# Kernel optimization log

Hardware: AMD Instinct MI355X
Metric: run time of the kernel (lower is better)

The kernel has to match this reference:

```python
import jax, jax.numpy as jnp
import numpy as np

L, B, S, H = 13, 32, 128, 768   # encoder hidden states: layers, batch (hardcoded 32), seq, hidden
U = 32                          # num_gru_units
G = 2 * U                       # linear out dim / bidirectional GRU feature dim (64)
NL = 2                          # num_labels
EPS = 1e-3                      # keras LayerNormalization default epsilon


def setup_inputs() -> dict:
    key = jax.random.key(0)
    ks = jax.random.split(key, 10)
    def n(k, shape, scale=0.05):
        return (jax.random.normal(k, shape, jnp.float32) * scale).astype(jnp.float32)
    return {
        "xs": jax.random.normal(ks[0], (L, B, S, H), jnp.float32),
        "W_lin": n(ks[1], (H, G)),
        "b_lin": jnp.zeros((G,), jnp.float32),
        "ln_gamma": jnp.ones((G,), jnp.float32),
        "ln_beta": jnp.zeros((G,), jnp.float32),
        "Wk_f": n(ks[2], (G, 3 * U)),
        "Wr_f": n(ks[3], (U, 3 * U)),
        "b_f": jnp.zeros((2, 3 * U), jnp.float32),   # [input_bias, recurrent_bias] (reset_after=True)
        "Wk_b": n(ks[4], (G, 3 * U)),
        "Wr_b": n(ks[5], (U, 3 * U)),
        "b_b": jnp.zeros((2, 3 * U), jnp.float32),
        "W_cls": n(ks[6], (G, NL)),
        "b_cls": jnp.zeros((NL,), jnp.float32),
    }


def _layernorm(x, g, b):
    m = jnp.mean(x, axis=-1, keepdims=True)
    v = jnp.var(x, axis=-1, keepdims=True)
    return (x - m) * jax.lax.rsqrt(v + EPS) * g + b


def _gru_dir(seq, h0, Wk, Wr, bias):
    # Keras GRU v2 cell (reset_after=True). seq: [B,S,G], h0: [B,U]
    xp = jnp.einsum('bsg,gk->bsk', seq, Wk) + bias[0]  # [B,S,3U]
    def step(h, x_t):
        rec = h @ Wr + bias[1]                          # [B,3U]
        z = jax.nn.sigmoid(x_t[:, :U] + rec[:, :U])
        r = jax.nn.sigmoid(x_t[:, U:2 * U] + rec[:, U:2 * U])
        hh = jnp.tanh(x_t[:, 2 * U:] + r * rec[:, 2 * U:])
        hn = z * h + (1.0 - z) * hh
        return hn, hn
    hT, ys = jax.lax.scan(step, h0, jnp.swapaxes(xp, 0, 1))  # scan over time
    return jnp.swapaxes(ys, 0, 1), hT                        # [B,S,U], [B,U]


def reference(xs, W_lin, b_lin, ln_gamma, ln_beta,
              Wk_f, Wr_f, b_f, Wk_b, Wr_b, b_b, W_cls, b_cls):
    # _forward: loop over the 13 encoder hidden-state layers; the bidirectional
    # GRU output feeds back as a residual into the next layer's linear output.
    # Dropout layers are treated as identity (deterministic reference), under
    # which the 100-pass MC average equals a single pass.
    seq = jnp.zeros((B, S, G), xs.dtype)  # initial 'sequence' of zeros
    h1 = jnp.zeros((B, U), xs.dtype)      # initial_state=None -> zeros in keras
    h2 = jnp.zeros((B, U), xs.dtype)
    for i in range(L):
        x = _layernorm(xs[i] @ W_lin + b_lin + seq, ln_gamma, ln_beta)  # [B,S,G]
        out_f, h1 = _gru_dir(x, h1, Wk_f, Wr_f, b_f)
        out_b, h2 = _gru_dir(x[:, ::-1], h2, Wk_b, Wr_b, b_b)
        seq = jnp.concatenate([out_f, out_b[:, ::-1]], axis=-1)         # [B,S,2U]
    # tf.stack([h1,h2], -1) -> [B,U,2]; reshape [32,-1] interleaves fwd/bwd units
    hcat = jnp.stack([h1, h2], axis=-1).reshape(B, -1)                  # [B,2U]
    return jax.nn.softmax(hcat @ W_cls + b_cls, axis=-1)                # [B,NL]
```

## Files before the change

### kernel.cpp

```cpp
#include <hip/hip_runtime.h>
#include <hip/hip_fp16.h>

#define L_ 13
#define B_ 32
#define S_ 128
#define H_ 768
#define NU 32
#define GG 64
#define TU 96
#define LN_EPS 1e-3f
#define SEQ_ST 68
#define XT_ST 129
#define WK_ST 100
#define XPH_ST 100
#define K1f 1.4426950408889634f
#define K2f 2.8853900817779268f

#define DPP_X1  0xB1
#define DPP_X2  0x4E
#define DPP_X7  0x141
#define DPP_X15 0x140

typedef float v2f __attribute__((ext_vector_type(2)));
typedef _Float16 h2t __attribute__((ext_vector_type(2)));
typedef unsigned int uv2 __attribute__((ext_vector_type(2)));

union F4H8 { float4 f4; __half2 hh[4]; h2t h[4]; };
union FH2  { float f; __half2 hh; h2t h; };
union F2H2 { float2 f2; __half2 hh[2]; };

__device__ __forceinline__ void pkfma(v2f& a, v2f x, v2f w) {
    asm("v_pk_fma_f32 %0, %1, %2, %0" : "+v"(a) : "v"(x), "v"(w));
}
template <int CTRL>
__device__ __forceinline__ float dppf(float x) {
    return __int_as_float(__builtin_amdgcn_update_dpp(
        0, __float_as_int(x), CTRL, 0xF, 0xF, true));
}
__device__ __forceinline__ float pairsum16(float x) {
#if __has_builtin(__builtin_amdgcn_permlane16_swap)
    uv2 s = __builtin_amdgcn_permlane16_swap(
        __float_as_uint(x), __float_as_uint(x), false, false);
    return __uint_as_float(s.x) + __uint_as_float(s.y);
#else
    return x + __shfl_xor(x, 16);
#endif
}
__device__ __forceinline__ void poll_ge_dev(unsigned* p, unsigned tgt) {
    int gd = 0;
    while (__hip_atomic_load(p, __ATOMIC_ACQUIRE, __HIP_MEMORY_SCOPE_AGENT) < tgt) {
        __builtin_amdgcn_s_sleep(2);
        if (++gd > (1 << 22)) break;
    }
}

__global__ __launch_bounds__(512) void fused_kernel(
    const float* __restrict__ xs, const float* __restrict__ Wl,
    const float* __restrict__ bl,
    __half* __restrict__ lin_all, unsigned* __restrict__ lincnt,
    const float* __restrict__ Wr_f, const float* __restrict__ b_f,
    const float* __restrict__ Wr_b, const float* __restrict__ b_b,
    const float* __restrict__ Wk_f, const float* __restrict__ Wk_b,
    const float* __restrict__ ln_g, const float* __restrict__ ln_b,
    const float* __restrict__ W_cls, const float* __restrict__ b_cls,
    float* __restrict__ out)
{
    extern __shared__ float sm[];
    const int bid = blockIdx.x;
    const int t = threadIdx.x;

    if (bid >= B_) {
        const int tix = bid - B_;
        const int l = tix >> 5;
        const int bb = tix & 31;
        const size_t row0 = (size_t)(l * B_ + bb) * S_;
        __half2* sA2 = (__half2*)sm;
        __half2* sW2 = (__half2*)(sm + 32 * 132);

        const int rgrp = t & 31;
        const int cg = t >> 5;
        const int c0 = cg * 4;

        float acc[4][4];
        #pragma unroll
        for (int i = 0; i < 4; ++i)
            #pragma unroll
            for (int j = 0; j < 4; ++j) acc[i][j] = 0.f;

        for (int kt = 0; kt < H_; kt += 64) {
            #pragma unroll
            for (int i = 0; i < 4; ++i) {
                const int idx = t + 512 * i;
                const int r = idx >> 4, kq = idx & 15;
                float4 a = *(const float4*)&xs[(row0 + r) * H_ + kt + kq * 4];
                sA2[(2 * kq) * 132 + r]     = __floats2half2_rn(a.x, a.y);
                sA2[(2 * kq + 1) * 132 + r] = __floats2half2_rn(a.z, a.w);
            }
            {
                const int k2 = t >> 4, c4 = (t & 15) * 4;
                float4 w0 = *(const float4*)&Wl[(size_t)(kt + 2 * k2) * GG + c4];
                float4 w1 = *(const float4*)&Wl[(size_t)(kt + 2 * k2 + 1) * GG + c4];
                sW2[k2 * 68 + c4 + 0] = __floats2half2_rn(w0.x, w1.x);
                sW2[k2 * 68 + c4 + 1] = __floats2half2_rn(w0.y, w1.y);
                sW2[k2 * 68 + c4 + 2] = __floats2half2_rn(w0.z, w1.z);
                sW2[k2 * 68 + c4 + 3] = __floats2half2_rn(w0.w, w1.w);
            }
            __syncthreads();
            #pragma unroll 4
            for (int k2 = 0; k2 < 32; ++k2) {
                FH2 x0, x1, x2, x3;
                x0.hh = sA2[k2 * 132 + rgrp];
                x1.hh = sA2[k2 * 132 + rgrp + 32];
                x2.hh = sA2[k2 * 132 + rgrp + 64];
                x3.hh = sA2[k2 * 132 + rgrp + 96];
                F4H8 w; w.f4 = *(const float4*)&sW2[k2 * 68 + c0];
                #pragma unroll
                for (int m = 0; m < 4; ++m) {
                    acc[0][m] = __builtin_amdgcn_fdot2(x0.h, w.h[m], acc[0][m], false);
                    acc[1][m] = __builtin_amdgcn_fdot2(x1.h, w.h[m], acc[1][m], false);
                    acc[2][m] = __builtin_amdgcn_fdot2(x2.h, w.h[m], acc[2][m], false);
                    acc[3][m] = __builtin_amdgcn_fdot2(x3.h, w.h[m], acc[3][m], false);
                }
            }
            __syncthreads();
        }
        const float4 bv = *(const float4*)&bl[c0];
        #pragma unroll
        for (int i = 0; i < 4; ++i) {
            const int r = rgrp + 32 * i;
            F2H2 u;
            u.hh[0] = __floats2half2_rn(acc[i][0] + bv.x, acc[i][1] + bv.y);
            u.hh[1] = __floats2half2_rn(acc[i][2] + bv.z, acc[i][3] + bv.w);
            *(float2*)&lin_all[(row0 + r) * GG + c0] = u.f2;
        }
        __threadfence();
        __syncthreads();
        if (t == 0)
            __hip_atomic_fetch_add(&lincnt[l], 1u, __ATOMIC_RELEASE, __HIP_MEMORY_SCOPE_AGENT);
        return;
    }

    float*   seqb = sm;
    __half2* xt2  = (__half2*)(sm + 8704);
    __half2* wk2  = (__half2*)(sm + 8704 + 4128);
    __half*  xph  = (__half*)(sm + 8704 + 4128 + 6400);
    float*   hbf  = sm + 8704 + 4128 + 6400 + 12800;
    float*   hbb  = hbf + NU;

    const int b = bid;
    const int wave = t >> 6;
    const int lane = t & 63;
    const int v16 = lane & 15;
    const int b4 = (lane >> 4) & 1;
    const int b5 = (lane >> 5) & 1;
    const int ud = v16 + 16 * b5;

    for (int i = t; i < S_ * SEQ_ST; i += 512) seqb[i] = 0.f;
    for (int i = t; i < 2 * 32 * 96; i += 512) {
        const int d = i / 3072, rem = i - d * 3072, k2 = rem / 96, c = rem - k2 * 96;
        const float* W = d ? Wk_b : Wk_f;
        const float sc = (c >= 64) ? K2f : K1f;
        wk2[(d * 32 + k2) * WK_ST + c] =
            __floats2half2_rn(W[(2 * k2) * TU + c] * sc, W[(2 * k2 + 1) * TU + c] * sc);
    }

    v2f wz[8], wr_[8], wh[8];
    float h_store = 0.f, h_dot = 0.f, rbz2 = 0.f, rbr2 = 0.f, rbh2 = 0.f;
    if (wave < 2) {
        const float* Wr   = wave ? Wr_b : Wr_f;
        const float* bias = wave ? b_b  : b_f;
        const int ex[8] = {0, 2, 7, 5, 15, 13, 8, 10};
        const int ey[8] = {1, 3, 6, 4, 14, 12, 9, 11};
        const int BB = 16 * b4;
        #pragma unroll
        for (int m = 0; m < 8; ++m) {
            const int jx = BB + (v16 ^ ex[m]), jy = BB + (v16 ^ ey[m]);
            wz[m]  = v2f{ K1f * Wr[jx * TU + ud],          K1f * Wr[jy * TU + ud] };
            wr_[m] = v2f{ K1f * Wr[jx * TU + NU + ud],     K1f * Wr[jy * TU + NU + ud] };
            wh[m]  = v2f{ K2f * Wr[jx * TU + 2 * NU + ud], K2f * Wr[jy * TU + 2 * NU + ud] };
        }
        rbz2 = 0.5f * K1f * bias[TU + ud];
        rbr2 = 0.5f * K1f * bias[TU + NU + ud];
        rbh2 = 0.5f * K2f * bias[TU + 2 * NU + ud];
    }

    const int g8 = t >> 3;
    const int c8 = (t & 7) << 3;
    const int rgrp = t & 31;
    const int cg = t >> 5;
    const int dsel = cg >> 3;
    const int cc = (cg & 7) * 12;
    const float* bias0 = dsel ? b_b : b_f;
    const __half2* wkd = wk2 + dsel * 32 * WK_ST;
    __half* xpd = xph + dsel * (S_ * XPH_ST);
    float bsc[12];
    #pragma unroll
    for (int m = 0; m < 12; ++m)
        bsc[m] = bias0[cc + m] * ((cc + m >= 64) ? K2f : K1f);

    __syncthreads();

    for (int l = 0; l < L_; ++l) {
        const __half* linb = lin_all + (size_t)(l * B_ + b) * S_ * GG;

        if (t == 0) poll_ge_dev(&lincnt[l], 32u);
        __syncthreads();

        #pragma unroll
        for (int p = 0; p < 2; ++p) {
            const int r = g8 + 64 * p;
            F4H8 lu; lu.f4 = *(const float4*)&linb[(size_t)r * GG + c8];
            float4 s0 = *(const float4*)&seqb[r * SEQ_ST + c8];
            float4 s1 = *(const float4*)&seqb[r * SEQ_ST + c8 + 4];
            float2 l0 = __half22float2(lu.hh[0]);
            float2 l1 = __half22float2(lu.hh[1]);
            float2 l2 = __half22float2(lu.hh[2]);
            float2 l3 = __half22float2(lu.hh[3]);
            float v[8];
            v[0] = l0.x + s0.x; v[1] = l0.y + s0.y; v[2] = l1.x + s0.z; v[3] = l1.y + s0.w;
            v[4] = l2.x + s1.x; v[5] = l2.y + s1.y; v[6] = l3.x + s1.z; v[7] = l3.y + s1.w;
            float s = 0.f;
            #pragma unroll
            for (int j = 0; j < 8; ++j) s += v[j];
            #pragma unroll
            for (int off = 1; off < 8; off <<= 1) s += __shfl_xor(s, off);
            const float mean = s * 0.015625f;
            float q = 0.f;
            float d[8];
            #pragma unroll
            for (int j = 0; j < 8; ++j) { d[j] = v[j] - mean; q += d[j] * d[j]; }
            #pragma unroll
            for (int off = 1; off < 8; off <<= 1) q += __shfl_xor(q, off);
            const float rstd = rsqrtf(q * 0.015625f + LN_EPS);
            float4 g0 = *(const float4*)&ln_g[c8];
            float4 g1 = *(const float4*)&ln_g[c8 + 4];
            float4 b0 = *(const float4*)&ln_b[c8];
            float4 b1 = *(const float4*)&ln_b[c8 + 4];
            float x[8];
            x[0] = d[0] * rstd * g0.x + b0.x; x[1] = d[1] * rstd * g0.y + b0.y;
            x[2] = d[2] * rstd * g0.z + b0.z; x[3] = d[3] * rstd * g0.w + b0.w;
            x[4] = d[4] * rstd * g1.x + b1.x; x[5] = d[5] * rstd * g1.y + b1.y;
            x[6] = d[6] * rstd * g1.z + b1.z; x[7] = d[7] * rstd * g1.w + b1.w;
            #pragma unroll
            for (int j = 0; j < 4; ++j)
                xt2[(c8 / 2 + j) * XT_ST + r] = __floats2half2_rn(x[2 * j], x[2 * j + 1]);
        }
        __syncthreads();

        {
            float acc[4][12];
            #pragma unroll
            for (int m = 0; m < 12; ++m) {
                acc[0][m] = bsc[m]; acc[1][m] = bsc[m]; acc[2][m] = bsc[m]; acc[3][m] = bsc[m];
            }
            #pragma unroll 4
            for (int k2 = 0; k2 < 32; ++k2) {
                FH2 x0, x1, x2, x3;
                x0.hh = xt2[k2 * XT_ST + rgrp];
                x1.hh = xt2[k2 * XT_ST + rgrp + 32];
                x2.hh = xt2[k2 * XT_ST + rgrp + 64];
                x3.hh = xt2[k2 * XT_ST + rgrp + 96];
                F4H8 wa, wb, wc;
                wa.f4 = *(const float4*)&wkd[k2 * WK_ST + cc];
                wb.f4 = *(const float4*)&wkd[k2 * WK_ST + cc + 4];
                wc.f4 = *(const float4*)&wkd[k2 * WK_ST + cc + 8];
                #pragma unroll
                for (int m = 0; m < 4; ++m) {
                    acc[0][m]     = __builtin_amdgcn_fdot2(x0.h, wa.h[m], acc[0][m],     false);
                    acc[1][m]     = __builtin_amdgcn_fdot2(x1.h, wa.h[m], acc[1][m],     false);
                    acc[2][m]     = __builtin_amdgcn_fdot2(x2.h, wa.h[m], acc[2][m],     false);
                    acc[3][m]     = __builtin_amdgcn_fdot2(x3.h, wa.h[m], acc[3][m],     false);
                    acc[0][m + 4] = __builtin_amdgcn_fdot2(x0.h, wb.h[m], acc[0][m + 4], false);
                    acc[1][m + 4] = __builtin_amdgcn_fdot2(x1.h, wb.h[m], acc[1][m + 4], false);
                    acc[2][m + 4] = __builtin_amdgcn_fdot2(x2.h, wb.h[m], acc[2][m + 4], false);
                    acc[3][m + 4] = __builtin_amdgcn_fdot2(x3.h, wb.h[m], acc[3][m + 4], false);
                    acc[0][m + 8] = __builtin_amdgcn_fdot2(x0.h, wc.h[m], acc[0][m + 8], false);
                    acc[1][m + 8] = __builtin_amdgcn_fdot2(x1.h, wc.h[m], acc[1][m + 8], false);
                    acc[2][m + 8] = __builtin_amdgcn_fdot2(x2.h, wc.h[m], acc[2][m + 8], false);
                    acc[3][m + 8] = __builtin_amdgcn_fdot2(x3.h, wc.h[m], acc[3][m + 8], false);
                }
            }
            #pragma unroll
            for (int i = 0; i < 4; ++i) {
                const int r = rgrp + 32 * i;
                __half2* dst = (__half2*)&xpd[r * XPH_ST + cc];
                #pragma unroll
                for (int j = 0; j < 6; ++j)
                    dst[j] = __floats2half2_rn(acc[i][2 * j], acc[i][2 * j + 1]);
            }
        }
        __syncthreads();

        if (wave < 2) {
            const int dir = wave;
            const __half* xp = xph + dir * (S_ * XPH_ST);
            float* sq = seqb + dir * NU + (lane & 31);
            const int stp = dir ? -1 : 1;
            int s = dir ? (S_ - 1) : 0;
            const bool wl = (lane < 32);
            const bool fix = (b4 != b5);
            float xz = (float)xp[s * XPH_ST + ud];
            float xr = (float)xp[s * XPH_ST + 32 + ud];
            float xh = (float)xp[s * XPH_ST + 64 + ud];
            for (int st = 0; st < S_; ++st) {
                float nz = 0.f, nr = 0.f, nh = 0.f;
                if (st < S_ - 1) {
                    const int sn = s + stp;
                    nz = (float)xp[sn * XPH_ST + ud];
                    nr = (float)xp[sn * XPH_ST + 32 + ud];
                    nh = (float)xp[sn * XPH_ST + 64 + ud];
                }
                v2f ro[8];
                ro[0].x = h_store;                ro[0].y = dppf<DPP_X1>(h_store);
                ro[1].x = dppf<DPP_X2>(ro[0].x);  ro[1].y = dppf<DPP_X2>(ro[0].y);
                ro[2].x = dppf<DPP_X7>(ro[0].x);  ro[2].y = dppf<DPP_X7>(ro[0].y);
                ro[3].x = dppf<DPP_X7>(ro[1].x);  ro[3].y = dppf<DPP_X7>(ro[1].y);
                ro[4].x = dppf<DPP_X15>(ro[0].x); ro[4].y = dppf<DPP_X15>(ro[0].y);
                ro[5].x = dppf<DPP_X15>(ro[1].x); ro[5].y = dppf<DPP_X15>(ro[1].y);
                ro[6].x = dppf<DPP_X15>(ro[2].x); ro[6].y = dppf<DPP_X15>(ro[2].y);
                ro[7].x = dppf<DPP_X15>(ro[3].x); ro[7].y = dppf<DPP_X15>(ro[3].y);

                v2f aza = v2f{0.5f * xz + rbz2, 0.f}, azb = v2f{0.f, 0.f};
                v2f ara = v2f{0.5f * xr + rbr2, 0.f}, arb = v2f{0.f, 0.f};
                v2f aha = v2f{rbh2, 0.f},             ahb = v2f{0.f, 0.f};
                #pragma unroll
                for (int m = 0; m < 4; ++m) {
                    pkfma(aza, ro[m], wz[m]);      pkfma(azb, ro[m + 4], wz[m + 4]);
                    pkfma(ara, ro[m], wr_[m]);     pkfma(arb, ro[m + 4], wr_[m + 4]);
                    pkfma(aha, ro[m], wh[m]);      pkfma(ahb, ro[m + 4], wh[m + 4]);
                }
                v2f azs = aza + azb, ars = ara + arb, ahs = aha + ahb;
                const float pz = pairsum16(azs.x + azs.y);
                const float pr = pairsum16(ars.x + ars.y);
                const float ph = pairsum16(ahs.x + ahs.y);

                const float z  = __builtin_amdgcn_rcpf(1.0f + __builtin_amdgcn_exp2f(-pz));
                const float r  = __builtin_amdgcn_rcpf(1.0f + __builtin_amdgcn_exp2f(-pr));
                const float tt = xh + r * ph;
                const float et = __builtin_amdgcn_exp2f(-tt);
                const float hh = (1.0f - et) * __builtin_amdgcn_rcpf(1.0f + et);
                const float hn_raw = hh + z * (h_dot - hh);
                h_dot = hn_raw;
                uv2 s32 = __builtin_amdgcn_permlane32_swap(
                    __float_as_uint(hn_raw), __float_as_uint(hn_raw), false, false);
                const float v32 = wl ? __uint_as_float(s32.y) : __uint_as_float(s32.x);
                h_store = fix ? v32 : hn_raw;
                if (wl) sq[s * SEQ_ST] = h_store;
                s += stp; xz = nz; xr = nr; xh = nh;
            }
        }
        __syncthreads();
    }

    if (wave < 2 && lane < 32) (wave ? hbb : hbf)[lane & 31] = h_store;
    __syncthreads();
    if (t == 0) {
        float l0 = b_cls[0], l1 = b_cls[1];
        for (int j = 0; j < NU; ++j) {
            const float hf = hbf[j], hk = hbb[j];
            l0 += hf * W_cls[4 * j]     + hk * W_cls[4 * j + 2];
            l1 += hf * W_cls[4 * j + 1] + hk * W_cls[4 * j + 3];
        }
        const float m = fmaxf(l0, l1);
        const float e0 = __expf(l0 - m), e1 = __expf(l1 - m);
        const float inv = 1.0f / (e0 + e1);
        out[b * 2 + 0] = e0 * inv;
        out[b * 2 + 1] = e1 * inv;
    }
}

extern "C" void kernel_launch(void* const* d_in, const int* in_sizes, int n_in,
                              void* d_out, int out_size, void* d_ws, size_t ws_size,
                              hipStream_t stream) {
    const float* xs    = (const float*)d_in[0];
    const float* W_lin = (const float*)d_in[1];
    const float* b_lin = (const float*)d_in[2];
    const float* ln_g  = (const float*)d_in[3];
    const float* ln_b  = (const float*)d_in[4];
    const float* Wk_f  = (const float*)d_in[5];
    const float* Wr_f  = (const float*)d_in[6];
    const float* b_f   = (const float*)d_in[7];
    const float* Wk_b  = (const float*)d_in[8];
    const float* Wr_b  = (const float*)d_in[9];
    const float* b_b   = (const float*)d_in[10];
    const float* W_cls = (const float*)d_in[11];
    const float* b_cls = (const float*)d_in[12];
    float* out = (float*)d_out;

    char* ws = (char*)d_ws;
    __half* lin_all = (__half*)ws;
    unsigned* lincnt = (unsigned*)(ws + 6815744);

    hipMemsetAsync(lincnt, 0, 64, stream);

    const int smem = (8704 + 4128 + 6400 + 12800 + 64) * (int)sizeof(float);
    (void)hipFuncSetAttribute((const void*)fused_kernel,
                              hipFuncAttributeMaxDynamicSharedMemorySize, smem);

    fused_kernel<<<B_ + L_ * B_, 512, smem, stream>>>(
        xs, W_lin, b_lin, lin_all, lincnt,
        Wr_f, b_f, Wr_b, b_b, Wk_f, Wk_b, ln_g, ln_b, W_cls, b_cls, out);
}
```

Baseline: 613.5 us.

## Split fused producer/consumer kernel into separate linear and GRU-chain launches

Replaces the single persistent kernel, whose extra blocks computed the input projection and signalled per-layer counters that the GRU blocks polled, with two launches: a projection kernel over all layers, then the recurrent chain kernel. This removes the atomic polling, the counter memset and the fences, and the projection blocks no longer compete with the 32 chain blocks for resources. In exchange, the chain can no longer start layer 0 while later layers' projections are still being computed, so that overlap is lost and the full projection cost sits on the critical path.

```diff
diff --git a/kernel.cpp b/kernel.cpp
--- a/kernel.cpp
+++ b/kernel.cpp
@@ -46,18 +46,77 @@
     return x + __shfl_xor(x, 16);
 #endif
 }
-__device__ __forceinline__ void poll_ge_dev(unsigned* p, unsigned tgt) {
-    int gd = 0;
-    while (__hip_atomic_load(p, __ATOMIC_ACQUIRE, __HIP_MEMORY_SCOPE_AGENT) < tgt) {
-        __builtin_amdgcn_s_sleep(2);
-        if (++gd > (1 << 22)) break;
-    }
-}
-
-__global__ __launch_bounds__(512) void fused_kernel(
+
+__global__ __launch_bounds__(512) void lin2_kernel(
     const float* __restrict__ xs, const float* __restrict__ Wl,
-    const float* __restrict__ bl,
-    __half* __restrict__ lin_all, unsigned* __restrict__ lincnt,
+    const float* __restrict__ bl, __half* __restrict__ lin_all)
+{
+    __shared__ __half2 sA2[32 * 132];
+    __shared__ __half2 sW2[32 * 68];
+
+    const int tix = blockIdx.x;
+    const size_t row0 = (size_t)tix * S_;
+    const int t = threadIdx.x;
+    const int rgrp = t & 31;
+    const int cg = t >> 5;
+    const int c0 = cg * 4;
+
+    float acc[4][4];
+    #pragma unroll
+    for (int i = 0; i < 4; ++i)
+        #pragma unroll
+        for (int j = 0; j < 4; ++j) acc[i][j] = 0.f;
+
+    for (int kt = 0; kt < H_; kt += 64) {
+        #pragma unroll
+        for (int i = 0; i < 4; ++i) {
+            const int idx = t + 512 * i;
+            const int r = idx >> 4, kq = idx & 15;
+            float4 a = *(const float4*)&xs[(row0 + r) * H_ + kt + kq * 4];
+            sA2[(2 * kq) * 132 + r]     = __floats2half2_rn(a.x, a.y);
+            sA2[(2 * kq + 1) * 132 + r] = __floats2half2_rn(a.z, a.w);
+        }
+        {
+            const int k2 = t >> 4, c4 = (t & 15) * 4;
+            float4 w0 = *(const float4*)&Wl[(size_t)(kt + 2 * k2) * GG + c4];
+            float4 w1 = *(const float4*)&Wl[(size_t)(kt + 2 * k2 + 1) * GG + c4];
+            sW2[k2 * 68 + c4 + 0] = __floats2half2_rn(w0.x, w1.x);
+            sW2[k2 * 68 + c4 + 1] = __floats2half2_rn(w0.y, w1.y);
+            sW2[k2 * 68 + c4 + 2] = __floats2half2_rn(w0.z, w1.z);
+            sW2[k2 * 68 + c4 + 3] = __floats2half2_rn(w0.w, w1.w);
+        }
+        __syncthreads();
+        #pragma unroll 4
+        for (int k2 = 0; k2 < 32; ++k2) {
+            FH2 x0, x1, x2, x3;
+            x0.hh = sA2[k2 * 132 + rgrp];
+            x1.hh = sA2[k2 * 132 + rgrp + 32];
+            x2.hh = sA2[k2 * 132 + rgrp + 64];
+            x3.hh = sA2[k2 * 132 + rgrp + 96];
+            F4H8 w; w.f4 = *(const float4*)&sW2[k2 * 68 + c0];
+            #pragma unroll
+            for (int m = 0; m < 4; ++m) {
+                acc[0][m] = __builtin_amdgcn_fdot2(x0.h, w.h[m], acc[0][m], false);
+                acc[1][m] = __builtin_amdgcn_fdot2(x1.h, w.h[m], acc[1][m], false);
+                acc[2][m] = __builtin_amdgcn_fdot2(x2.h, w.h[m], acc[2][m], false);
+                acc[3][m] = __builtin_amdgcn_fdot2(x3.h, w.h[m], acc[3][m], false);
+            }
+        }
+        __syncthreads();
+    }
+    const float4 bv = *(const float4*)&bl[c0];
+    #pragma unroll
+    for (int i = 0; i < 4; ++i) {
+        const int r = rgrp + 32 * i;
+        F2H2 u;
+        u.hh[0] = __floats2half2_rn(acc[i][0] + bv.x, acc[i][1] + bv.y);
+        u.hh[1] = __floats2half2_rn(acc[i][2] + bv.z, acc[i][3] + bv.w);
+        *(float2*)&lin_all[(row0 + r) * GG + c0] = u.f2;
+    }
+}
+
+__global__ __launch_bounds__(512) void chain_kernel(
+    const __half* __restrict__ lin_all,
     const float* __restrict__ Wr_f, const float* __restrict__ b_f,
     const float* __restrict__ Wr_b, const float* __restrict__ b_b,
     const float* __restrict__ Wk_f, const float* __restrict__ Wk_b,
@@ -66,80 +125,6 @@
     float* __restrict__ out)
 {
     extern __shared__ float sm[];
-    const int bid = blockIdx.x;
-    const int t = threadIdx.x;
-
-    if (bid >= B_) {
-        const int tix = bid - B_;
-        const int l = tix >> 5;
-        const int bb = tix & 31;
-        const size_t row0 = (size_t)(l * B_ + bb) * S_;
-        __half2* sA2 = (__half2*)sm;
-        __half2* sW2 = (__half2*)(sm + 32 * 132);
-
-        const int rgrp = t & 31;
-        const int cg = t >> 5;
-        const int c0 = cg * 4;
-
-        float acc[4][4];
-        #pragma unroll
-        for (int i = 0; i < 4; ++i)
-            #pragma unroll
-            for (int j = 0; j < 4; ++j) acc[i][j] = 0.f;
-
-        for (int kt = 0; kt < H_; kt += 64) {
-            #pragma unroll
-            for (int i = 0; i < 4; ++i) {
-                const int idx = t + 512 * i;
-                const int r = idx >> 4, kq = idx & 15;
-                float4 a = *(const float4*)&xs[(row0 + r) * H_ + kt + kq * 4];
-                sA2[(2 * kq) * 132 + r]     = __floats2half2_rn(a.x, a.y);
-                sA2[(2 * kq + 1) * 132 + r] = __floats2half2_rn(a.z, a.w);
-            }
-            {
-                const int k2 = t >> 4, c4 = (t & 15) * 4;
-                float4 w0 = *(const float4*)&Wl[(size_t)(kt + 2 * k2) * GG + c4];
-                float4 w1 = *(const float4*)&Wl[(size_t)(kt + 2 * k2 + 1) * GG + c4];
-                sW2[k2 * 68 + c4 + 0] = __floats2half2_rn(w0.x, w1.x);
-                sW2[k2 * 68 + c4 + 1] = __floats2half2_rn(w0.y, w1.y);
-                sW2[k2 * 68 + c4 + 2] = __floats2half2_rn(w0.z, w1.z);
-                sW2[k2 * 68 + c4 + 3] = __floats2half2_rn(w0.w, w1.w);
-            }
-            __syncthreads();
-            #pragma unroll 4
-            for (int k2 = 0; k2 < 32; ++k2) {
-                FH2 x0, x1, x2, x3;
-                x0.hh = sA2[k2 * 132 + rgrp];
-                x1.hh = sA2[k2 * 132 + rgrp + 32];
-                x2.hh = sA2[k2 * 132 + rgrp + 64];
-                x3.hh = sA2[k2 * 132 + rgrp + 96];
-                F4H8 w; w.f4 = *(const float4*)&sW2[k2 * 68 + c0];
-                #pragma unroll
-                for (int m = 0; m < 4; ++m) {
-                    acc[0][m] = __builtin_amdgcn_fdot2(x0.h, w.h[m], acc[0][m], false);
-                    acc[1][m] = __builtin_amdgcn_fdot2(x1.h, w.h[m], acc[1][m], false);
-                    acc[2][m] = __builtin_amdgcn_fdot2(x2.h, w.h[m], acc[2][m], false);
-                    acc[3][m] = __builtin_amdgcn_fdot2(x3.h, w.h[m], acc[3][m], false);
-                }
-            }
-            __syncthreads();
-        }
-        const float4 bv = *(const float4*)&bl[c0];
-        #pragma unroll
-        for (int i = 0; i < 4; ++i) {
-            const int r = rgrp + 32 * i;
-            F2H2 u;
-            u.hh[0] = __floats2half2_rn(acc[i][0] + bv.x, acc[i][1] + bv.y);
-            u.hh[1] = __floats2half2_rn(acc[i][2] + bv.z, acc[i][3] + bv.w);
-            *(float2*)&lin_all[(row0 + r) * GG + c0] = u.f2;
-        }
-        __threadfence();
-        __syncthreads();
-        if (t == 0)
-            __hip_atomic_fetch_add(&lincnt[l], 1u, __ATOMIC_RELEASE, __HIP_MEMORY_SCOPE_AGENT);
-        return;
-    }
-
     float*   seqb = sm;
     __half2* xt2  = (__half2*)(sm + 8704);
     __half2* wk2  = (__half2*)(sm + 8704 + 4128);
@@ -147,7 +132,8 @@
     float*   hbf  = sm + 8704 + 4128 + 6400 + 12800;
     float*   hbb  = hbf + NU;
 
-    const int b = bid;
+    const int b = blockIdx.x;
+    const int t = threadIdx.x;
     const int wave = t >> 6;
     const int lane = t & 63;
     const int v16 = lane & 15;
@@ -202,9 +188,6 @@
 
     for (int l = 0; l < L_; ++l) {
         const __half* linb = lin_all + (size_t)(l * B_ + b) * S_ * GG;
-
-        if (t == 0) poll_ge_dev(&lincnt[l], 32u);
-        __syncthreads();
 
         #pragma unroll
         for (int p = 0; p < 2; ++p) {
@@ -387,17 +370,14 @@
     const float* b_cls = (const float*)d_in[12];
     float* out = (float*)d_out;
 
-    char* ws = (char*)d_ws;
-    __half* lin_all = (__half*)ws;
-    unsigned* lincnt = (unsigned*)(ws + 6815744);
-
-    hipMemsetAsync(lincnt, 0, 64, stream);
+    __half* lin_all = (__half*)d_ws;
 
     const int smem = (8704 + 4128 + 6400 + 12800 + 64) * (int)sizeof(float);
-    (void)hipFuncSetAttribute((const void*)fused_kernel,
+    (void)hipFuncSetAttribute((const void*)chain_kernel,
                               hipFuncAttributeMaxDynamicSharedMemorySize, smem);
 
-    fused_kernel<<<B_ + L_ * B_, 512, smem, stream>>>(
-        xs, W_lin, b_lin, lin_all, lincnt,
-        Wr_f, b_f, Wr_b, b_b, Wk_f, Wk_b, ln_g, ln_b, W_cls, b_cls, out);
-}
+    lin2_kernel<<<L_ * B_, 512, 0, stream>>>(xs, W_lin, b_lin, lin_all);
+
+    chain_kernel<<<B_, 512, smem, stream>>>(
+        lin_all, Wr_f, b_f, Wr_b, b_b, Wk_f, Wk_b, ln_g, ln_b, W_cls, b_cls, out);
+}
```

Measured after the change: 587.8 us, median of 2. 4.2% less time.
